# Optimization experiments

Hardware: AMD Instinct MI355X
Metric: run time of the kernel (lower is better)

Reference implementation:

```python
import jax, jax.numpy as jnp
import numpy as np
import math

L_MAX = 8  # matches init_kwargs max_angular
N_PAIR = 1_000_000


def setup_inputs() -> dict:
    key = jax.random.key(0)
    R = jax.random.normal(key, (N_PAIR, 3), dtype=jnp.float32)
    return {"R": R}


def _solid_harmonics(R, l_max):
    """Real solid harmonics r^l * Y_l^m (Wikipedia convention, sphericart math).

    Returns a tuple of arrays, one per l, each of shape [N, 2l+1], with m
    ordered -l..l (sin terms, m=0, cos terms).
    """
    x, y, z = R[:, 0], R[:, 1], R[:, 2]
    r2 = x * x + y * y + z * z
    one = jnp.ones_like(x)

    # c_m + i s_m = (x + i y)^m  ->  c_m = r_xy^m cos(m phi), s_m = r_xy^m sin(m phi)
    c = [one]
    s = [jnp.zeros_like(x)]
    for m in range(1, l_max + 1):
        c.append(x * c[m - 1] - y * s[m - 1])
        s.append(x * s[m - 1] + y * c[m - 1])

    # Q_l^m(z, r): r^{l-m} * (associated-Legendre part), via degree recurrence.
    # Q_l^l = -(2l-1) Q_{l-1}^{l-1};  Q_l^{l-1} = (2l-1) z Q_{l-1}^{l-1};
    # Q_l^m = ((2l-1) z Q_{l-1}^m - (l+m-1) r^2 Q_{l-2}^m) / (l-m)
    Q = {(0, 0): one}
    for l in range(1, l_max + 1):
        Q[(l, l)] = -(2 * l - 1) * Q[(l - 1, l - 1)]
        Q[(l, l - 1)] = (2 * l - 1) * z * Q[(l - 1, l - 1)]
        for m in range(l - 2, -1, -1):
            Q[(l, m)] = ((2 * l - 1) * z * Q[(l - 1, m)]
                         - (l + m - 1) * r2 * Q[(l - 2, m)]) / (l - m)

    def F(l, m):
        # (-1)^m cancels the Condon-Shortley phase inside Q -> Wikipedia convention
        return ((-1.0) ** m) * math.sqrt(
            (2 * l + 1) / (2 * math.pi)
            * math.factorial(l - m) / math.factorial(l + m))

    out = []
    for l in range(l_max + 1):
        cols = []
        for m in range(l, 0, -1):           # m = -l .. -1 (sin branch)
            cols.append(F(l, m) * Q[(l, m)] * s[m])
        cols.append(math.sqrt((2 * l + 1) / (4 * math.pi)) * Q[(l, 0)])  # m = 0
        for m in range(1, l + 1):           # m = 1 .. l (cos branch)
            cols.append(F(l, m) * Q[(l, m)] * c[m])
        out.append(jnp.stack(cols, axis=-1))  # [N, 2l+1]
    return tuple(out)


def reference(R):
    # Mirrors SolidHarmonics.forward: expansion split per degree l.
    return _solid_harmonics(R, L_MAX)
```

## Files before the change

### kernel.cpp

```cpp
#include <hip/hip_runtime.h>
#include <math.h>

#define LMAX 8

struct Coefs {
    float F[LMAX + 1][LMAX + 1];
    float A[LMAX + 1][LMAX + 1];
    float B[LMAX + 1][LMAX + 1];
};

__global__ __launch_bounds__(256) void solid_harmonics_kernel(
    const float* __restrict__ R, float* __restrict__ out, int N, Coefs cf)
{
    int i = blockIdx.x * blockDim.x + threadIdx.x;
    if (i >= N) return;

    float x = R[3 * i + 0];
    float y = R[3 * i + 1];
    float z = R[3 * i + 2];
    float r2 = x * x + y * y + z * z;

    float c[LMAX + 1], s[LMAX + 1];
    c[0] = 1.0f; s[0] = 0.0f;
#pragma unroll
    for (int m = 1; m <= LMAX; ++m) {
        c[m] = x * c[m - 1] - y * s[m - 1];
        s[m] = x * s[m - 1] + y * c[m - 1];
    }

    float Q[LMAX + 1][LMAX + 1];
    Q[0][0] = 1.0f;
#pragma unroll
    for (int l = 1; l <= LMAX; ++l) {
        Q[l][l]     = -(2.0f * l - 1.0f) * Q[l - 1][l - 1];
        Q[l][l - 1] =  (2.0f * l - 1.0f) * z * Q[l - 1][l - 1];
#pragma unroll
        for (int m = l - 2; m >= 0; --m) {
            Q[l][m] = cf.A[l][m] * z * Q[l - 1][m] - cf.B[l][m] * r2 * Q[l - 2][m];
        }
    }

#pragma unroll
    for (int l = 0; l <= LMAX; ++l) {
        float* o = out + (size_t)N * (size_t)(l * l) + (size_t)i * (size_t)(2 * l + 1);
#pragma unroll
        for (int m = l; m >= 1; --m) {
            o[l - m] = cf.F[l][m] * Q[l][m] * s[m];
        }
        o[l] = cf.F[l][0] * Q[l][0];
#pragma unroll
        for (int m = 1; m <= l; ++m) {
            o[l + m] = cf.F[l][m] * Q[l][m] * c[m];
        }
    }
}

extern "C" void kernel_launch(void* const* d_in, const int* in_sizes, int n_in,
                              void* d_out, int out_size, void* d_ws, size_t ws_size,
                              hipStream_t stream) {
    const float* R = (const float*)d_in[0];
    float* out = (float*)d_out;
    const int N = in_sizes[0] / 3;

    Coefs cf;
    double fact[2 * LMAX + 1];
    fact[0] = 1.0;
    for (int k = 1; k <= 2 * LMAX; ++k) fact[k] = fact[k - 1] * (double)k;
    const double PI = 3.14159265358979323846;
    for (int l = 0; l <= LMAX; ++l) {
        cf.F[l][0] = (float)sqrt((2.0 * l + 1.0) / (4.0 * PI));
        for (int m = 1; m <= l; ++m) {
            double sign = (m & 1) ? -1.0 : 1.0;
            cf.F[l][m] = (float)(sign * sqrt((2.0 * l + 1.0) / (2.0 * PI)
                                             * fact[l - m] / fact[l + m]));
        }
        for (int m = 0; m <= l - 2; ++m) {
            cf.A[l][m] = (float)((2.0 * l - 1.0) / (double)(l - m));
            cf.B[l][m] = (float)((double)(l + m - 1) / (double)(l - m));
        }
    }
    for (int l = 0; l <= LMAX; ++l)
        for (int m = 0; m <= LMAX; ++m) {
            if (m > l) { cf.F[l][m] = 0.f; }
            if (m > l - 2) { cf.A[l][m] = 0.f; cf.B[l][m] = 0.f; }
        }

    const int block = 256;
    const int grid = (N + block - 1) / block;
    solid_harmonics_kernel<<<grid, block, 0, stream>>>(R, out, N, cf);
}
```

Baseline: 360.2 us.

## Stage per-degree outputs in shared memory for coalesced vectorized stores

Each thread writes its 2l+1 harmonics for degree l into a shared-memory tile. After a barrier, the block copies the contiguous output chunk to global memory with float4 stores where the address is aligned. The old code made strided per-thread scalar stores, which coalesce poorly. The Q recurrence now keeps only three rolling rows to reduce register pressure, at the cost of two barriers per degree and extra shared-memory traffic.

```diff
diff --git a/kernel.cpp b/kernel.cpp
--- a/kernel.cpp
+++ b/kernel.cpp
@@ -1,7 +1,9 @@
 #include <hip/hip_runtime.h>
 #include <math.h>
+#include <stdint.h>
 
 #define LMAX 8
+#define NPB 256
 
 struct Coefs {
     float F[LMAX + 1][LMAX + 1];
@@ -12,46 +14,70 @@
 __global__ __launch_bounds__(256) void solid_harmonics_kernel(
     const float* __restrict__ R, float* __restrict__ out, int N, Coefs cf)
 {
-    int i = blockIdx.x * blockDim.x + threadIdx.x;
-    if (i >= N) return;
+    __shared__ __align__(16) float tile[NPB * (2 * LMAX + 1)];
 
-    float x = R[3 * i + 0];
-    float y = R[3 * i + 1];
-    float z = R[3 * i + 2];
-    float r2 = x * x + y * y + z * z;
+    const int t = threadIdx.x;
+    const int i0 = blockIdx.x * NPB;
+    const int i = i0 + t;
+    const int rows = min(NPB, N - i0);
+    const bool valid = (i < N);
+
+    float x = 0.f, y = 0.f, z = 0.f;
+    if (valid) {
+        x = R[3 * i + 0];
+        y = R[3 * i + 1];
+        z = R[3 * i + 2];
+    }
+    const float r2 = x * x + y * y + z * z;
 
     float c[LMAX + 1], s[LMAX + 1];
-    c[0] = 1.0f; s[0] = 0.0f;
-#pragma unroll
-    for (int m = 1; m <= LMAX; ++m) {
-        c[m] = x * c[m - 1] - y * s[m - 1];
-        s[m] = x * s[m - 1] + y * c[m - 1];
-    }
+    c[0] = 1.f; s[0] = 0.f;
 
-    float Q[LMAX + 1][LMAX + 1];
-    Q[0][0] = 1.0f;
-#pragma unroll
-    for (int l = 1; l <= LMAX; ++l) {
-        Q[l][l]     = -(2.0f * l - 1.0f) * Q[l - 1][l - 1];
-        Q[l][l - 1] =  (2.0f * l - 1.0f) * z * Q[l - 1][l - 1];
-#pragma unroll
-        for (int m = l - 2; m >= 0; --m) {
-            Q[l][m] = cf.A[l][m] * z * Q[l - 1][m] - cf.B[l][m] * r2 * Q[l - 2][m];
-        }
-    }
+    float Qcur[LMAX + 1], Qm1[LMAX + 1], Qm2[LMAX + 1];
+    Qcur[0] = 1.f;
 
 #pragma unroll
     for (int l = 0; l <= LMAX; ++l) {
-        float* o = out + (size_t)N * (size_t)(l * l) + (size_t)i * (size_t)(2 * l + 1);
+        if (l >= 1) {
 #pragma unroll
-        for (int m = l; m >= 1; --m) {
-            o[l - m] = cf.F[l][m] * Q[l][m] * s[m];
+            for (int m = 0; m < l - 1; ++m) Qm2[m] = Qm1[m];
+#pragma unroll
+            for (int m = 0; m < l; ++m) Qm1[m] = Qcur[m];
+            c[l] = x * c[l - 1] - y * s[l - 1];
+            s[l] = x * s[l - 1] + y * c[l - 1];
+            Qcur[l]     = -(2.f * l - 1.f) * Qm1[l - 1];
+            Qcur[l - 1] =  (2.f * l - 1.f) * z * Qm1[l - 1];
+#pragma unroll
+            for (int m = l - 2; m >= 0; --m)
+                Qcur[m] = cf.A[l][m] * z * Qm1[m] - cf.B[l][m] * r2 * Qm2[m];
         }
-        o[l] = cf.F[l][0] * Q[l][0];
+
+        const int stride = 2 * l + 1;
+
+        {
+            float* row = &tile[t * stride];
 #pragma unroll
-        for (int m = 1; m <= l; ++m) {
-            o[l + m] = cf.F[l][m] * Q[l][m] * c[m];
+            for (int m = l; m >= 1; --m) row[l - m] = cf.F[l][m] * Qcur[m] * s[m];
+            row[l] = cf.F[l][0] * Qcur[0];
+#pragma unroll
+            for (int m = 1; m <= l; ++m) row[l + m] = cf.F[l][m] * Qcur[m] * c[m];
         }
+        __syncthreads();
+
+        {
+            float* obase = out + (size_t)N * (size_t)(l * l) + (size_t)i0 * (size_t)stride;
+            const int E = rows * stride;
+            if ((((uintptr_t)obase) & 15u) == 0) {
+                const int E4 = E >> 2;
+                const float4* t4 = (const float4*)tile;
+                float4* o4 = (float4*)obase;
+                for (int e = t; e < E4; e += NPB) o4[e] = t4[e];
+                for (int e = (E4 << 2) + t; e < E; e += NPB) obase[e] = tile[e];
+            } else {
+                for (int e = t; e < E; e += NPB) obase[e] = tile[e];
+            }
+        }
+        __syncthreads();
     }
 }
 
@@ -68,6 +94,7 @@
     for (int k = 1; k <= 2 * LMAX; ++k) fact[k] = fact[k - 1] * (double)k;
     const double PI = 3.14159265358979323846;
     for (int l = 0; l <= LMAX; ++l) {
+        for (int m = 0; m <= LMAX; ++m) { cf.F[l][m] = 0.f; cf.A[l][m] = 0.f; cf.B[l][m] = 0.f; }
         cf.F[l][0] = (float)sqrt((2.0 * l + 1.0) / (4.0 * PI));
         for (int m = 1; m <= l; ++m) {
             double sign = (m & 1) ? -1.0 : 1.0;
@@ -79,13 +106,8 @@
             cf.B[l][m] = (float)((double)(l + m - 1) / (double)(l - m));
         }
     }
-    for (int l = 0; l <= LMAX; ++l)
-        for (int m = 0; m <= LMAX; ++m) {
-            if (m > l) { cf.F[l][m] = 0.f; }
-            if (m > l - 2) { cf.A[l][m] = 0.f; cf.B[l][m] = 0.f; }
-        }
 
-    const int block = 256;
+    const int block = NPB;
     const int grid = (N + block - 1) / block;
     solid_harmonics_kernel<<<grid, block, 0, stream>>>(R, out, N, cf);
 }
```

New measurement: 328.4 us. 1.1x faster.
